# Optimization experiments

Measured on AMD Instinct MI355X. Metric: run time of the kernel, lower is better.

Reference implementation:

```python
import jax, jax.numpy as jnp
import numpy as np

N, E = 10000, 320000
IN_CH, HID, HEADS, OUT_CH = 128, 64, 4, 64
NEG_SLOPE = 0.2


def gat_conv(x, edge_index, edge_attr, W, a_src, a_dst, a_edge, W_edge, bias,
             heads, out_ch, concat):
    """PyG-style GATConv with edge_dim features.
    x: [N, F_in], edge_index: [2, E] (row0=src, row1=dst), edge_attr: [E, edge_dim].
    W: [F_in, heads*out_ch], a_*: [heads, out_ch], W_edge: [edge_dim, heads*out_ch],
    bias: [heads*out_ch] if concat else [out_ch].
    """
    n = x.shape[0]
    xh = (x @ W).reshape(n, heads, out_ch)                       # [N,H,C]
    src, dst = edge_index[0], edge_index[1]
    al_s = jnp.einsum('nhc,hc->nh', xh, a_src)                   # [N,H]
    al_d = jnp.einsum('nhc,hc->nh', xh, a_dst)                   # [N,H]
    eh = (edge_attr @ W_edge).reshape(-1, heads, out_ch)         # [E,H,C]
    al_e = jnp.einsum('ehc,hc->eh', eh, a_edge)                  # [E,H]
    alpha = jax.nn.leaky_relu(al_s[src] + al_d[dst] + al_e, NEG_SLOPE)  # [E,H]
    # segment softmax over incoming edges of each destination node
    amax = jax.ops.segment_max(alpha, dst, num_segments=n)       # [N,H]
    amax = jax.lax.stop_gradient(jnp.where(jnp.isfinite(amax), amax, 0.0))
    ex = jnp.exp(alpha - amax[dst])
    denom = jax.ops.segment_sum(ex, dst, num_segments=n)         # [N,H]
    att = ex / (denom[dst] + 1e-16)                              # [E,H]
    out = jax.ops.segment_sum(xh[src] * att[:, :, None], dst, num_segments=n)  # [N,H,C]
    out = out.reshape(n, heads * out_ch) if concat else out.mean(axis=1)
    return out + bias


def setup_inputs() -> dict:
    key = jax.random.key(0)
    ks = jax.random.split(key, 16)
    s1 = 1.0 / np.sqrt(IN_CH)
    s2 = 1.0 / np.sqrt(HEADS * HID)
    return {
        'x': jax.random.normal(ks[0], (N, IN_CH), dtype=jnp.float32),
        'edge_weight': jax.random.uniform(ks[1], (E, 1), dtype=jnp.float32),
        'W1': jax.random.normal(ks[2], (IN_CH, HEADS * HID), dtype=jnp.float32) * s1,
        'a_src1': jax.random.normal(ks[3], (HEADS, HID), dtype=jnp.float32) * s2,
        'a_dst1': jax.random.normal(ks[4], (HEADS, HID), dtype=jnp.float32) * s2,
        'a_edge1': jax.random.normal(ks[5], (HEADS, HID), dtype=jnp.float32) * s2,
        'We1': jax.random.normal(ks[6], (1, HEADS * HID), dtype=jnp.float32),
        'b1': jnp.zeros((HEADS * HID,), dtype=jnp.float32),
        'W2': jax.random.normal(ks[7], (HEADS * HID, OUT_CH), dtype=jnp.float32) * s2,
        'a_src2': jax.random.normal(ks[8], (1, OUT_CH), dtype=jnp.float32) * s2,
        'a_dst2': jax.random.normal(ks[9], (1, OUT_CH), dtype=jnp.float32) * s2,
        'a_edge2': jax.random.normal(ks[10], (1, OUT_CH), dtype=jnp.float32) * s2,
        'We2': jax.random.normal(ks[11], (1, OUT_CH), dtype=jnp.float32),
        'b2': jnp.zeros((OUT_CH,), dtype=jnp.float32),
        'edge_index': jax.random.randint(ks[12], (2, E), 0, N, dtype=jnp.int64
                                         if jax.config.jax_enable_x64 else jnp.int32),
    }


def reference(x, edge_weight, W1, a_src1, a_dst1, a_edge1, We1, b1,
              W2, a_src2, a_dst2, a_edge2, We2, b2, edge_index):
    h = gat_conv(x, edge_index, edge_weight, W1, a_src1, a_dst1, a_edge1, We1, b1,
                 heads=HEADS, out_ch=HID, concat=True)
    h = jax.nn.elu(h)
    out = gat_conv(h, edge_index, edge_weight, W2, a_src2, a_dst2, a_edge2, We2, b2,
                   heads=1, out_ch=OUT_CH, concat=False)
    return out
```

## Files before the change

kernel.cpp:

```cpp
#include <hip/hip_runtime.h>

constexpr int N_NODES = 10000;
constexpr int N_EDGES = 320000;
constexpr int IN_CH   = 128;
constexpr int HID     = 64;
constexpr int HEADS   = 4;
constexpr int OUT_CH  = 64;
constexpr int F1      = HEADS * HID;
constexpr int CAP     = 128;
constexpr float NEG_SLOPE = 0.2f;
constexpr int GEMM_BLOCKS = (N_NODES + 31) / 32;
constexpr int HALF_E = N_EDGES / 2;


__global__ void k_init(int* __restrict__ cnt,
                       const float* __restrict__ We1, const float* __restrict__ ae1,
                       const float* __restrict__ We2, const float* __restrict__ ae2,
                       float* __restrict__ de) {
    int bid = blockIdx.x;
    if (bid < 40) {
        int i = bid * 256 + threadIdx.x;
        if (i < N_NODES) cnt[i] = 0;
        return;
    }
    int t = threadIdx.x;
    if (t < HEADS) {
        float s = 0.f;
        for (int c = 0; c < HID; ++c) s = fmaf(We1[t * HID + c], ae1[t * HID + c], s);
        de[t] = s;
    } else if (t == HEADS) {
        float s = 0.f;
        for (int c = 0; c < OUT_CH; ++c) s = fmaf(We2[c], ae2[c], s);
        de[HEADS] = s;
    }
}


__global__ __launch_bounds__(256) void k_gemm1(const float* __restrict__ x,
                                               const float* __restrict__ W,
                                               const float* __restrict__ a_src,
                                               const float* __restrict__ a_dst,
                                               float* __restrict__ xh1T,
                                               float* __restrict__ als4,
                                               float* __restrict__ ald4) {
    __shared__ float xs[32 * IN_CH];
    int tid = threadIdx.x;
    int row0 = blockIdx.x * 32;
    int nrows = N_NODES - row0; if (nrows > 32) nrows = 32;
    float4* xs4 = (float4*)xs;
    const float4* xg = (const float4*)(x + (size_t)row0 * IN_CH);
    #pragma unroll
    for (int j = 0; j < 4; ++j) {
        int idx = tid + j * 256;
        if ((idx >> 5) < nrows) xs4[idx] = xg[idx];
    }
    __syncthreads();
    int wv = tid >> 6;
    int lane = tid & 63;
    int col = lane * 4;
    int h = lane >> 4;
    int c = (lane & 15) * 4;
    float acc[8][4];
    #pragma unroll
    for (int m = 0; m < 8; ++m)
        #pragma unroll
        for (int j = 0; j < 4; ++j) acc[m][j] = 0.f;

    for (int k = 0; k < IN_CH; k += 4) {
        float4 w0 = *(const float4*)(W + (size_t)(k + 0) * F1 + col);
        float4 w1 = *(const float4*)(W + (size_t)(k + 1) * F1 + col);
        float4 w2 = *(const float4*)(W + (size_t)(k + 2) * F1 + col);
        float4 w3 = *(const float4*)(W + (size_t)(k + 3) * F1 + col);
        #pragma unroll
        for (int m = 0; m < 8; ++m) {
            float4 xv = *(const float4*)(xs + (wv * 8 + m) * IN_CH + k);
            acc[m][0] = fmaf(xv.x, w0.x, fmaf(xv.y, w1.x, fmaf(xv.z, w2.x, fmaf(xv.w, w3.x, acc[m][0]))));
            acc[m][1] = fmaf(xv.x, w0.y, fmaf(xv.y, w1.y, fmaf(xv.z, w2.y, fmaf(xv.w, w3.y, acc[m][1]))));
            acc[m][2] = fmaf(xv.x, w0.z, fmaf(xv.y, w1.z, fmaf(xv.z, w2.z, fmaf(xv.w, w3.z, acc[m][2]))));
            acc[m][3] = fmaf(xv.x, w0.w, fmaf(xv.y, w1.w, fmaf(xv.z, w2.w, fmaf(xv.w, w3.w, acc[m][3]))));
        }
    }
    float4 asv = *(const float4*)(a_src + h * HID + c);
    float4 adv = *(const float4*)(a_dst + h * HID + c);
    #pragma unroll
    for (int m = 0; m < 8; ++m) {
        int row = wv * 8 + m;
        if (row < nrows)
            *(float4*)(xh1T + ((size_t)h * N_NODES + row0 + row) * HID + c) = *(float4*)acc[m];
        float s = acc[m][0] * asv.x + acc[m][1] * asv.y + acc[m][2] * asv.z + acc[m][3] * asv.w;
        float d = acc[m][0] * adv.x + acc[m][1] * adv.y + acc[m][2] * adv.z + acc[m][3] * adv.w;
        #pragma unroll
        for (int off = 1; off < 16; off <<= 1) {
            s += __shfl_xor(s, off, 64);
            d += __shfl_xor(d, off, 64);
        }
        if ((lane & 15) == 0 && row < nrows) {
            als4[(size_t)(row0 + row) * HEADS + h] = s;
            ald4[(size_t)(row0 + row) * HEADS + h] = d;
        }
    }
}


__global__ void k_fill(const int* __restrict__ src, const int* __restrict__ dst,
                       const float* __restrict__ ew,
                       const float* __restrict__ als4, const float* __restrict__ ald4,
                       const float* __restrict__ de, int* __restrict__ cnt,
                       int2* __restrict__ sw_pad, float4* __restrict__ ex_pad4) {
    int e0 = blockIdx.x * 256 + threadIdx.x;
    int e1 = e0 + HALF_E;
    int s0 = src[e0], d0 = dst[e0];
    int s1 = src[e1], d1 = dst[e1];
    float w0 = ew[e0], w1 = ew[e1];
    int p0 = atomicAdd(&cnt[d0], 1);
    int p1 = atomicAdd(&cnt[d1], 1);
    float4 as0 = *(const float4*)(als4 + (size_t)s0 * HEADS);
    float4 as1 = *(const float4*)(als4 + (size_t)s1 * HEADS);
    float4 ad0 = *(const float4*)(ald4 + (size_t)d0 * HEADS);
    float4 ad1 = *(const float4*)(ald4 + (size_t)d1 * HEADS);
    float4 dv = *(const float4*)de;
    if (p0 < CAP) {
        size_t q = (size_t)d0 * CAP + p0;
        sw_pad[q] = make_int2(s0, __float_as_int(w0));
        float4 a;
        a.x = as0.x + ad0.x + w0 * dv.x;
        a.y = as0.y + ad0.y + w0 * dv.y;
        a.z = as0.z + ad0.z + w0 * dv.z;
        a.w = as0.w + ad0.w + w0 * dv.w;
        a.x = a.x > 0.f ? a.x : NEG_SLOPE * a.x;
        a.y = a.y > 0.f ? a.y : NEG_SLOPE * a.y;
        a.z = a.z > 0.f ? a.z : NEG_SLOPE * a.z;
        a.w = a.w > 0.f ? a.w : NEG_SLOPE * a.w;
        a.x = __expf(a.x); a.y = __expf(a.y); a.z = __expf(a.z); a.w = __expf(a.w);
        ex_pad4[q] = a;
    }
    if (p1 < CAP) {
        size_t q = (size_t)d1 * CAP + p1;
        sw_pad[q] = make_int2(s1, __float_as_int(w1));
        float4 a;
        a.x = as1.x + ad1.x + w1 * dv.x;
        a.y = as1.y + ad1.y + w1 * dv.y;
        a.z = as1.z + ad1.z + w1 * dv.z;
        a.w = as1.w + ad1.w + w1 * dv.w;
        a.x = a.x > 0.f ? a.x : NEG_SLOPE * a.x;
        a.y = a.y > 0.f ? a.y : NEG_SLOPE * a.y;
        a.z = a.z > 0.f ? a.z : NEG_SLOPE * a.z;
        a.w = a.w > 0.f ? a.w : NEG_SLOPE * a.w;
        a.x = __expf(a.x); a.y = __expf(a.y); a.z = __expf(a.z); a.w = __expf(a.w);
        ex_pad4[q] = a;
    }
}


__global__ __launch_bounds__(256) void k_agg1(
        const float* __restrict__ xh1T, const float4* __restrict__ ex_pad4,
        const int2* __restrict__ sw_pad, const int* __restrict__ cnt,
        const float* __restrict__ bias, float* __restrict__ h1) {
    int b = blockIdx.x;
    int slot8 = b & 7;
    int h = slot8 >> 1;
    int nb = (b >> 3) * 2 + (slot8 & 1);
    int node = nb * 4 + (threadIdx.x >> 6);
    int lane = threadIdx.x & 63;
    int es = lane >> 4;
    int c4 = (lane & 15) * 4;
    const float* xb  = xh1T + (size_t)h * N_NODES * HID;
    const float* exb = (const float*)(ex_pad4 + (size_t)node * CAP) + h;
    const int2*  sp  = sw_pad + (size_t)node * CAP;
    int n = cnt[node]; if (n > CAP) n = CAP;
    float4 acc = make_float4(0.f, 0.f, 0.f, 0.f);
    float den = 0.f;
    int i = es;
    for (; i + 4 < n; i += 8) {
        float e0 = exb[i * 4], e1 = exb[(i + 4) * 4];
        int s0 = sp[i].x, s1 = sp[i + 4].x;
        float4 x0 = *(const float4*)(xb + (size_t)s0 * HID + c4);
        float4 x1 = *(const float4*)(xb + (size_t)s1 * HID + c4);
        den += e0 + e1;
        acc.x = fmaf(e0, x0.x, fmaf(e1, x1.x, acc.x));
        acc.y = fmaf(e0, x0.y, fmaf(e1, x1.y, acc.y));
        acc.z = fmaf(e0, x0.z, fmaf(e1, x1.z, acc.z));
        acc.w = fmaf(e0, x0.w, fmaf(e1, x1.w, acc.w));
    }
    if (i < n) {
        float e0 = exb[i * 4];
        int s0 = sp[i].x;
        float4 x0 = *(const float4*)(xb + (size_t)s0 * HID + c4);
        den += e0;
        acc.x = fmaf(e0, x0.x, acc.x);
        acc.y = fmaf(e0, x0.y, acc.y);
        acc.z = fmaf(e0, x0.z, acc.z);
        acc.w = fmaf(e0, x0.w, acc.w);
    }
    #pragma unroll
    for (int off = 32; off >= 16; off >>= 1) {
        acc.x += __shfl_xor(acc.x, off, 64);
        acc.y += __shfl_xor(acc.y, off, 64);
        acc.z += __shfl_xor(acc.z, off, 64);
        acc.w += __shfl_xor(acc.w, off, 64);
        den   += __shfl_xor(den,   off, 64);
    }
    if (es == 0) {
        float inv = 1.f / (den + 1e-16f);
        int cb = h * HID + c4;
        float4 o;
        o.x = fmaf(acc.x, inv, bias[cb + 0]);
        o.y = fmaf(acc.y, inv, bias[cb + 1]);
        o.z = fmaf(acc.z, inv, bias[cb + 2]);
        o.w = fmaf(acc.w, inv, bias[cb + 3]);
        o.x = o.x > 0.f ? o.x : expm1f(o.x);
        o.y = o.y > 0.f ? o.y : expm1f(o.y);
        o.z = o.z > 0.f ? o.z : expm1f(o.z);
        o.w = o.w > 0.f ? o.w : expm1f(o.w);
        *(float4*)(h1 + (size_t)node * F1 + cb) = o;
    }
}


__global__ __launch_bounds__(256) void k_gemm2(const float* __restrict__ hin,
                                               const float* __restrict__ W,
                                               const float* __restrict__ a_src,
                                               const float* __restrict__ a_dst,
                                               float* __restrict__ xh2,
                                               float* __restrict__ als,
                                               float* __restrict__ ald) {
    __shared__ float hs[32 * F1];
    int tid = threadIdx.x;
    int row0 = blockIdx.x * 32;
    int nrows = N_NODES - row0; if (nrows > 32) nrows = 32;
    float4* hs4 = (float4*)hs;
    const float4* hg = (const float4*)(hin + (size_t)row0 * F1);
    #pragma unroll
    for (int j = 0; j < 8; ++j) {
        int idx = tid + j * 256;
        if ((idx >> 6) < nrows) hs4[idx] = hg[idx];
    }
    __syncthreads();
    int rowg = tid >> 4;
    int col = (tid & 15) * 4;
    float acc[2][4];
    #pragma unroll
    for (int m = 0; m < 2; ++m)
        #pragma unroll
        for (int j = 0; j < 4; ++j) acc[m][j] = 0.f;
    for (int k = 0; k < F1; k += 4) {
        float4 w0 = *(const float4*)(W + (size_t)(k + 0) * OUT_CH + col);
        float4 w1 = *(const float4*)(W + (size_t)(k + 1) * OUT_CH + col);
        float4 w2 = *(const float4*)(W + (size_t)(k + 2) * OUT_CH + col);
        float4 w3 = *(const float4*)(W + (size_t)(k + 3) * OUT_CH + col);
        #pragma unroll
        for (int m = 0; m < 2; ++m) {
            float4 xv = *(const float4*)(hs + (rowg * 2 + m) * F1 + k);
            acc[m][0] = fmaf(xv.x, w0.x, fmaf(xv.y, w1.x, fmaf(xv.z, w2.x, fmaf(xv.w, w3.x, acc[m][0]))));
            acc[m][1] = fmaf(xv.x, w0.y, fmaf(xv.y, w1.y, fmaf(xv.z, w2.y, fmaf(xv.w, w3.y, acc[m][1]))));
            acc[m][2] = fmaf(xv.x, w0.z, fmaf(xv.y, w1.z, fmaf(xv.z, w2.z, fmaf(xv.w, w3.z, acc[m][2]))));
            acc[m][3] = fmaf(xv.x, w0.w, fmaf(xv.y, w1.w, fmaf(xv.z, w2.w, fmaf(xv.w, w3.w, acc[m][3]))));
        }
    }
    int lane = tid & 63;
    float4 asv = *(const float4*)(a_src + col);
    float4 adv = *(const float4*)(a_dst + col);
    #pragma unroll
    for (int m = 0; m < 2; ++m) {
        int row = rowg * 2 + m;
        if (row < nrows) *(float4*)(xh2 + (size_t)(row0 + row) * OUT_CH + col) = *(float4*)acc[m];
        float s = acc[m][0] * asv.x + acc[m][1] * asv.y + acc[m][2] * asv.z + acc[m][3] * asv.w;
        float d = acc[m][0] * adv.x + acc[m][1] * adv.y + acc[m][2] * adv.z + acc[m][3] * adv.w;
        #pragma unroll
        for (int off = 1; off < 16; off <<= 1) {
            s += __shfl_xor(s, off, 64);
            d += __shfl_xor(d, off, 64);
        }
        if ((lane & 15) == 0 && row < nrows) {
            als[row0 + row] = s;
            ald[row0 + row] = d;
        }
    }
}


__global__ __launch_bounds__(256) void k_agg2(
        const float* __restrict__ xh2, const float* __restrict__ als,
        const float* __restrict__ ald, const int2* __restrict__ sw_pad,
        const int* __restrict__ cnt, const float* __restrict__ de,
        const float* __restrict__ bias, float* __restrict__ out) {
    int node = blockIdx.x * 4 + (threadIdx.x >> 6);
    int lane = threadIdx.x & 63;
    int es = lane >> 4;
    int c4 = (lane & 15) * 4;
    float de2  = de[HEADS];
    float aldv = ald[node];
    const int2* sp = sw_pad + (size_t)node * CAP;
    int n = cnt[node]; if (n > CAP) n = CAP;
    float4 acc = make_float4(0.f, 0.f, 0.f, 0.f);
    float den = 0.f;
    int i = es;
    for (; i + 4 < n; i += 8) {
        int2 sw0 = sp[i], sw1 = sp[i + 4];
        int s0 = sw0.x, s1 = sw1.x;
        float w0 = __int_as_float(sw0.y), w1 = __int_as_float(sw1.y);
        float a0 = als[s0] + aldv + w0 * de2;
        float a1 = als[s1] + aldv + w1 * de2;
        a0 = a0 > 0.f ? a0 : NEG_SLOPE * a0;
        a1 = a1 > 0.f ? a1 : NEG_SLOPE * a1;
        float e0 = __expf(a0), e1 = __expf(a1);
        float4 x0 = *(const float4*)(xh2 + (size_t)s0 * OUT_CH + c4);
        float4 x1 = *(const float4*)(xh2 + (size_t)s1 * OUT_CH + c4);
        den += e0 + e1;
        acc.x = fmaf(e0, x0.x, fmaf(e1, x1.x, acc.x));
        acc.y = fmaf(e0, x0.y, fmaf(e1, x1.y, acc.y));
        acc.z = fmaf(e0, x0.z, fmaf(e1, x1.z, acc.z));
        acc.w = fmaf(e0, x0.w, fmaf(e1, x1.w, acc.w));
    }
    if (i < n) {
        int2 sw0 = sp[i];
        int s0 = sw0.x;
        float w0 = __int_as_float(sw0.y);
        float a0 = als[s0] + aldv + w0 * de2;
        a0 = a0 > 0.f ? a0 : NEG_SLOPE * a0;
        float e0 = __expf(a0);
        float4 x0 = *(const float4*)(xh2 + (size_t)s0 * OUT_CH + c4);
        den += e0;
        acc.x = fmaf(e0, x0.x, acc.x);
        acc.y = fmaf(e0, x0.y, acc.y);
        acc.z = fmaf(e0, x0.z, acc.z);
        acc.w = fmaf(e0, x0.w, acc.w);
    }
    #pragma unroll
    for (int off = 32; off >= 16; off >>= 1) {
        acc.x += __shfl_xor(acc.x, off, 64);
        acc.y += __shfl_xor(acc.y, off, 64);
        acc.z += __shfl_xor(acc.z, off, 64);
        acc.w += __shfl_xor(acc.w, off, 64);
        den   += __shfl_xor(den,   off, 64);
    }
    if (es == 0) {
        float inv = 1.f / (den + 1e-16f);
        float4 o;
        o.x = fmaf(acc.x, inv, bias[c4 + 0]);
        o.y = fmaf(acc.y, inv, bias[c4 + 1]);
        o.z = fmaf(acc.z, inv, bias[c4 + 2]);
        o.w = fmaf(acc.w, inv, bias[c4 + 3]);
        *(float4*)(out + (size_t)node * OUT_CH + c4) = o;
    }
}


extern "C" void kernel_launch(void* const* d_in, const int* in_sizes, int n_in,
                              void* d_out, int out_size, void* d_ws, size_t ws_size,
                              hipStream_t stream) {
    const float* x       = (const float*)d_in[0];
    const float* ew      = (const float*)d_in[1];
    const float* W1      = (const float*)d_in[2];
    const float* a_src1  = (const float*)d_in[3];
    const float* a_dst1  = (const float*)d_in[4];
    const float* a_edge1 = (const float*)d_in[5];
    const float* We1     = (const float*)d_in[6];
    const float* b1      = (const float*)d_in[7];
    const float* W2      = (const float*)d_in[8];
    const float* a_src2  = (const float*)d_in[9];
    const float* a_dst2  = (const float*)d_in[10];
    const float* a_edge2 = (const float*)d_in[11];
    const float* We2     = (const float*)d_in[12];
    const float* b2      = (const float*)d_in[13];
    const int*   eidx    = (const int*)d_in[14];
    const int* esrc = eidx;
    const int* edst = eidx + N_EDGES;
    float* out = (float*)d_out;

    char* p = (char*)d_ws;
    auto alloc = [&](size_t bytes) {
        char* r = p;
        p += (bytes + 255) & ~(size_t)255;
        return r;
    };
    float* xh1T     = (float*)alloc((size_t)N_NODES * F1 * 4);
    float* h1       = (float*)alloc((size_t)N_NODES * F1 * 4);
    float* xh2      = (float*)alloc((size_t)N_NODES * OUT_CH * 4);
    float* als4     = (float*)alloc((size_t)N_NODES * HEADS * 4);
    float* ald4     = (float*)alloc((size_t)N_NODES * HEADS * 4);
    float* als2     = (float*)alloc((size_t)N_NODES * 4);
    float* ald2     = (float*)alloc((size_t)N_NODES * 4);
    float* de       = (float*)alloc(8 * 4);
    int*   cnt      = (int*)alloc((size_t)N_NODES * 4);
    int2*  sw_pad   = (int2*)alloc((size_t)N_NODES * CAP * 8);
    float4* ex_pad4 = (float4*)alloc((size_t)N_NODES * CAP * 16);

    k_init<<<41, 256, 0, stream>>>(cnt, We1, a_edge1, We2, a_edge2, de);

    k_gemm1<<<GEMM_BLOCKS, 256, 0, stream>>>(x, W1, a_src1, a_dst1, xh1T, als4, ald4);

    k_fill<<<HALF_E / 256, 256, 0, stream>>>(esrc, edst, ew, als4, ald4, de,
                                             cnt, sw_pad, ex_pad4);

    k_agg1<<<N_NODES / 4 * HEADS, 256, 0, stream>>>(xh1T, ex_pad4, sw_pad, cnt, b1, h1);

    k_gemm2<<<GEMM_BLOCKS, 256, 0, stream>>>(h1, W2, a_src2, a_dst2, xh2, als2, ald2);
    k_agg2<<<N_NODES / 4, 256, 0, stream>>>(xh2, als2, ald2, sw_pad, cnt, de, b2, out);
}
```

Before: 121.7 us.

## Compute layer-1 attention exponentials inside aggregation instead of precomputing per edge

Result: no change. 121.7 us (+0.1%).

```diff
diff --git a/kernel.cpp b/kernel.cpp
--- a/kernel.cpp
+++ b/kernel.cpp
@@ -36,13 +36,28 @@
 }
 
 
+__global__ void k_fill(const int* __restrict__ src, const int* __restrict__ dst,
+                       const float* __restrict__ ew,
+                       int* __restrict__ cnt, int2* __restrict__ sw_pad) {
+    int e0 = blockIdx.x * 256 + threadIdx.x;
+    int e1 = e0 + HALF_E;
+    int s0 = src[e0], d0 = dst[e0];
+    int s1 = src[e1], d1 = dst[e1];
+    float w0 = ew[e0], w1 = ew[e1];
+    int p0 = atomicAdd(&cnt[d0], 1);
+    int p1 = atomicAdd(&cnt[d1], 1);
+    if (p0 < CAP) sw_pad[(size_t)d0 * CAP + p0] = make_int2(s0, __float_as_int(w0));
+    if (p1 < CAP) sw_pad[(size_t)d1 * CAP + p1] = make_int2(s1, __float_as_int(w1));
+}
+
+
 __global__ __launch_bounds__(256) void k_gemm1(const float* __restrict__ x,
                                                const float* __restrict__ W,
                                                const float* __restrict__ a_src,
                                                const float* __restrict__ a_dst,
                                                float* __restrict__ xh1T,
-                                               float* __restrict__ als4,
-                                               float* __restrict__ ald4) {
+                                               float* __restrict__ alsT,
+                                               float* __restrict__ aldT) {
     __shared__ float xs[32 * IN_CH];
     int tid = threadIdx.x;
     int row0 = blockIdx.x * 32;
@@ -95,66 +110,17 @@
             d += __shfl_xor(d, off, 64);
         }
         if ((lane & 15) == 0 && row < nrows) {
-            als4[(size_t)(row0 + row) * HEADS + h] = s;
-            ald4[(size_t)(row0 + row) * HEADS + h] = d;
-        }
-    }
-}
-
-
-__global__ void k_fill(const int* __restrict__ src, const int* __restrict__ dst,
-                       const float* __restrict__ ew,
-                       const float* __restrict__ als4, const float* __restrict__ ald4,
-                       const float* __restrict__ de, int* __restrict__ cnt,
-                       int2* __restrict__ sw_pad, float4* __restrict__ ex_pad4) {
-    int e0 = blockIdx.x * 256 + threadIdx.x;
-    int e1 = e0 + HALF_E;
-    int s0 = src[e0], d0 = dst[e0];
-    int s1 = src[e1], d1 = dst[e1];
-    float w0 = ew[e0], w1 = ew[e1];
-    int p0 = atomicAdd(&cnt[d0], 1);
-    int p1 = atomicAdd(&cnt[d1], 1);
-    float4 as0 = *(const float4*)(als4 + (size_t)s0 * HEADS);
-    float4 as1 = *(const float4*)(als4 + (size_t)s1 * HEADS);
-    float4 ad0 = *(const float4*)(ald4 + (size_t)d0 * HEADS);
-    float4 ad1 = *(const float4*)(ald4 + (size_t)d1 * HEADS);
-    float4 dv = *(const float4*)de;
-    if (p0 < CAP) {
-        size_t q = (size_t)d0 * CAP + p0;
-        sw_pad[q] = make_int2(s0, __float_as_int(w0));
-        float4 a;
-        a.x = as0.x + ad0.x + w0 * dv.x;
-        a.y = as0.y + ad0.y + w0 * dv.y;
-        a.z = as0.z + ad0.z + w0 * dv.z;
-        a.w = as0.w + ad0.w + w0 * dv.w;
-        a.x = a.x > 0.f ? a.x : NEG_SLOPE * a.x;
-        a.y = a.y > 0.f ? a.y : NEG_SLOPE * a.y;
-        a.z = a.z > 0.f ? a.z : NEG_SLOPE * a.z;
-        a.w = a.w > 0.f ? a.w : NEG_SLOPE * a.w;
-        a.x = __expf(a.x); a.y = __expf(a.y); a.z = __expf(a.z); a.w = __expf(a.w);
-        ex_pad4[q] = a;
-    }
-    if (p1 < CAP) {
-        size_t q = (size_t)d1 * CAP + p1;
-        sw_pad[q] = make_int2(s1, __float_as_int(w1));
-        float4 a;
-        a.x = as1.x + ad1.x + w1 * dv.x;
-        a.y = as1.y + ad1.y + w1 * dv.y;
-        a.z = as1.z + ad1.z + w1 * dv.z;
-        a.w = as1.w + ad1.w + w1 * dv.w;
-        a.x = a.x > 0.f ? a.x : NEG_SLOPE * a.x;
-        a.y = a.y > 0.f ? a.y : NEG_SLOPE * a.y;
-        a.z = a.z > 0.f ? a.z : NEG_SLOPE * a.z;
-        a.w = a.w > 0.f ? a.w : NEG_SLOPE * a.w;
-        a.x = __expf(a.x); a.y = __expf(a.y); a.z = __expf(a.z); a.w = __expf(a.w);
-        ex_pad4[q] = a;
+            alsT[(size_t)h * N_NODES + row0 + row] = s;
+            aldT[(size_t)h * N_NODES + row0 + row] = d;
+        }
     }
 }
 
 
 __global__ __launch_bounds__(256) void k_agg1(
-        const float* __restrict__ xh1T, const float4* __restrict__ ex_pad4,
-        const int2* __restrict__ sw_pad, const int* __restrict__ cnt,
+        const float* __restrict__ xh1T, const float* __restrict__ alsT,
+        const float* __restrict__ aldT, const int2* __restrict__ sw_pad,
+        const int* __restrict__ cnt, const float* __restrict__ de,
         const float* __restrict__ bias, float* __restrict__ h1) {
     int b = blockIdx.x;
     int slot8 = b & 7;
@@ -164,28 +130,44 @@
     int lane = threadIdx.x & 63;
     int es = lane >> 4;
     int c4 = (lane & 15) * 4;
-    const float* xb  = xh1T + (size_t)h * N_NODES * HID;
-    const float* exb = (const float*)(ex_pad4 + (size_t)node * CAP) + h;
-    const int2*  sp  = sw_pad + (size_t)node * CAP;
+    const float* xb   = xh1T + (size_t)h * N_NODES * HID;
+    const float* alsb = alsT + (size_t)h * N_NODES;
+    float deh  = de[h];
+    float aldv = aldT[(size_t)h * N_NODES + node];
+    const int2* sp = sw_pad + (size_t)node * CAP;
     int n = cnt[node]; if (n > CAP) n = CAP;
     float4 acc = make_float4(0.f, 0.f, 0.f, 0.f);
     float den = 0.f;
     int i = es;
-    for (; i + 4 < n; i += 8) {
-        float e0 = exb[i * 4], e1 = exb[(i + 4) * 4];
-        int s0 = sp[i].x, s1 = sp[i + 4].x;
-        float4 x0 = *(const float4*)(xb + (size_t)s0 * HID + c4);
-        float4 x1 = *(const float4*)(xb + (size_t)s1 * HID + c4);
-        den += e0 + e1;
-        acc.x = fmaf(e0, x0.x, fmaf(e1, x1.x, acc.x));
-        acc.y = fmaf(e0, x0.y, fmaf(e1, x1.y, acc.y));
-        acc.z = fmaf(e0, x0.z, fmaf(e1, x1.z, acc.z));
-        acc.w = fmaf(e0, x0.w, fmaf(e1, x1.w, acc.w));
-    }
-    if (i < n) {
-        float e0 = exb[i * 4];
-        int s0 = sp[i].x;
-        float4 x0 = *(const float4*)(xb + (size_t)s0 * HID + c4);
+    for (; i + 12 < n; i += 16) {
+        int2 r0 = sp[i], r1 = sp[i + 4], r2 = sp[i + 8], r3 = sp[i + 12];
+        float al0 = alsb[r0.x], al1 = alsb[r1.x], al2 = alsb[r2.x], al3 = alsb[r3.x];
+        float4 x0 = *(const float4*)(xb + (size_t)r0.x * HID + c4);
+        float4 x1 = *(const float4*)(xb + (size_t)r1.x * HID + c4);
+        float4 x2 = *(const float4*)(xb + (size_t)r2.x * HID + c4);
+        float4 x3 = *(const float4*)(xb + (size_t)r3.x * HID + c4);
+        float a0 = al0 + aldv + __int_as_float(r0.y) * deh;
+        float a1 = al1 + aldv + __int_as_float(r1.y) * deh;
+        float a2 = al2 + aldv + __int_as_float(r2.y) * deh;
+        float a3 = al3 + aldv + __int_as_float(r3.y) * deh;
+        a0 = a0 > 0.f ? a0 : NEG_SLOPE * a0;
+        a1 = a1 > 0.f ? a1 : NEG_SLOPE * a1;
+        a2 = a2 > 0.f ? a2 : NEG_SLOPE * a2;
+        a3 = a3 > 0.f ? a3 : NEG_SLOPE * a3;
+        float e0 = __expf(a0), e1 = __expf(a1), e2 = __expf(a2), e3 = __expf(a3);
+        den += (e0 + e1) + (e2 + e3);
+        acc.x = fmaf(e0, x0.x, fmaf(e1, x1.x, fmaf(e2, x2.x, fmaf(e3, x3.x, acc.x))));
+        acc.y = fmaf(e0, x0.y, fmaf(e1, x1.y, fmaf(e2, x2.y, fmaf(e3, x3.y, acc.y))));
+        acc.z = fmaf(e0, x0.z, fmaf(e1, x1.z, fmaf(e2, x2.z, fmaf(e3, x3.z, acc.z))));
+        acc.w = fmaf(e0, x0.w, fmaf(e1, x1.w, fmaf(e2, x2.w, fmaf(e3, x3.w, acc.w))));
+    }
+    for (; i < n; i += 4) {
+        int2 r0 = sp[i];
+        float al0 = alsb[r0.x];
+        float4 x0 = *(const float4*)(xb + (size_t)r0.x * HID + c4);
+        float a0 = al0 + aldv + __int_as_float(r0.y) * deh;
+        a0 = a0 > 0.f ? a0 : NEG_SLOPE * a0;
+        float e0 = __expf(a0);
         den += e0;
         acc.x = fmaf(e0, x0.x, acc.x);
         acc.y = fmaf(e0, x0.y, acc.y);
@@ -295,31 +277,35 @@
     float4 acc = make_float4(0.f, 0.f, 0.f, 0.f);
     float den = 0.f;
     int i = es;
-    for (; i + 4 < n; i += 8) {
-        int2 sw0 = sp[i], sw1 = sp[i + 4];
-        int s0 = sw0.x, s1 = sw1.x;
-        float w0 = __int_as_float(sw0.y), w1 = __int_as_float(sw1.y);
-        float a0 = als[s0] + aldv + w0 * de2;
-        float a1 = als[s1] + aldv + w1 * de2;
+    for (; i + 12 < n; i += 16) {
+        int2 r0 = sp[i], r1 = sp[i + 4], r2 = sp[i + 8], r3 = sp[i + 12];
+        float al0 = als[r0.x], al1 = als[r1.x], al2 = als[r2.x], al3 = als[r3.x];
+        float4 x0 = *(const float4*)(xh2 + (size_t)r0.x * OUT_CH + c4);
+        float4 x1 = *(const float4*)(xh2 + (size_t)r1.x * OUT_CH + c4);
+        float4 x2 = *(const float4*)(xh2 + (size_t)r2.x * OUT_CH + c4);
+        float4 x3 = *(const float4*)(xh2 + (size_t)r3.x * OUT_CH + c4);
+        float a0 = al0 + aldv + __int_as_float(r0.y) * de2;
+        float a1 = al1 + aldv + __int_as_float(r1.y) * de2;
+        float a2 = al2 + aldv + __int_as_float(r2.y) * de2;
+        float a3 = al3 + aldv + __int_as_float(r3.y) * de2;
         a0 = a0 > 0.f ? a0 : NEG_SLOPE * a0;
         a1 = a1 > 0.f ? a1 : NEG_SLOPE * a1;
-        float e0 = __expf(a0), e1 = __expf(a1);
-        float4 x0 = *(const float4*)(xh2 + (size_t)s0 * OUT_CH + c4);
-        float4 x1 = *(const float4*)(xh2 + (size_t)s1 * OUT_CH + c4);
-        den += e0 + e1;
-        acc.x = fmaf(e0, x0.x, fmaf(e1, x1.x, acc.x));
-        acc.y = fmaf(e0, x0.y, fmaf(e1, x1.y, acc.y));
-        acc.z = fmaf(e0, x0.z, fmaf(e1, x1.z, acc.z));
-        acc.w = fmaf(e0, x0.w, fmaf(e1, x1.w, acc.w));
-    }
-    if (i < n) {
-        int2 sw0 = sp[i];
-        int s0 = sw0.x;
-        float w0 = __int_as_float(sw0.y);
-        float a0 = als[s0] + aldv + w0 * de2;
+        a2 = a2 > 0.f ? a2 : NEG_SLOPE * a2;
+        a3 = a3 > 0.f ? a3 : NEG_SLOPE * a3;
+        float e0 = __expf(a0), e1 = __expf(a1), e2 = __expf(a2), e3 = __expf(a3);
+        den += (e0 + e1) + (e2 + e3);
+        acc.x = fmaf(e0, x0.x, fmaf(e1, x1.x, fmaf(e2, x2.x, fmaf(e3, x3.x, acc.x))));
+        acc.y = fmaf(e0, x0.y, fmaf(e1, x1.y, fmaf(e2, x2.y, fmaf(e3, x3.y, acc.y))));
+        acc.z = fmaf(e0, x0.z, fmaf(e1, x1.z, fmaf(e2, x2.z, fmaf(e3, x3.z, acc.z))));
+        acc.w = fmaf(e0, x0.w, fmaf(e1, x1.w, fmaf(e3, x3.w, fmaf(e2, x2.w, acc.w))));
+    }
+    for (; i < n; i += 4) {
+        int2 r0 = sp[i];
+        float al0 = als[r0.x];
+        float4 x0 = *(const float4*)(xh2 + (size_t)r0.x * OUT_CH + c4);
+        float a0 = al0 + aldv + __int_as_float(r0.y) * de2;
         a0 = a0 > 0.f ? a0 : NEG_SLOPE * a0;
         float e0 = __expf(a0);
-        float4 x0 = *(const float4*)(xh2 + (size_t)s0 * OUT_CH + c4);
         den += e0;
         acc.x = fmaf(e0, x0.x, acc.x);
         acc.y = fmaf(e0, x0.y, acc.y);
@@ -374,26 +360,25 @@
         p += (bytes + 255) & ~(size_t)255;
         return r;
     };
-    float* xh1T     = (float*)alloc((size_t)N_NODES * F1 * 4);
-    float* h1       = (float*)alloc((size_t)N_NODES * F1 * 4);
-    float* xh2      = (float*)alloc((size_t)N_NODES * OUT_CH * 4);
-    float* als4     = (float*)alloc((size_t)N_NODES * HEADS * 4);
-    float* ald4     = (float*)alloc((size_t)N_NODES * HEADS * 4);
-    float* als2     = (float*)alloc((size_t)N_NODES * 4);
-    float* ald2     = (float*)alloc((size_t)N_NODES * 4);
-    float* de       = (float*)alloc(8 * 4);
-    int*   cnt      = (int*)alloc((size_t)N_NODES * 4);
-    int2*  sw_pad   = (int2*)alloc((size_t)N_NODES * CAP * 8);
-    float4* ex_pad4 = (float4*)alloc((size_t)N_NODES * CAP * 16);
+    float* xh1T   = (float*)alloc((size_t)N_NODES * F1 * 4);
+    float* h1     = (float*)alloc((size_t)N_NODES * F1 * 4);
+    float* xh2    = (float*)alloc((size_t)N_NODES * OUT_CH * 4);
+    float* alsT   = (float*)alloc((size_t)N_NODES * HEADS * 4);
+    float* aldT   = (float*)alloc((size_t)N_NODES * HEADS * 4);
+    float* als2   = (float*)alloc((size_t)N_NODES * 4);
+    float* ald2   = (float*)alloc((size_t)N_NODES * 4);
+    float* de     = (float*)alloc(8 * 4);
+    int*   cnt    = (int*)alloc((size_t)N_NODES * 4);
+    int2*  sw_pad = (int2*)alloc((size_t)N_NODES * CAP * 8);
 
     k_init<<<41, 256, 0, stream>>>(cnt, We1, a_edge1, We2, a_edge2, de);
 
-    k_gemm1<<<GEMM_BLOCKS, 256, 0, stream>>>(x, W1, a_src1, a_dst1, xh1T, als4, ald4);
-
-    k_fill<<<HALF_E / 256, 256, 0, stream>>>(esrc, edst, ew, als4, ald4, de,
-                                             cnt, sw_pad, ex_pad4);
-
-    k_agg1<<<N_NODES / 4 * HEADS, 256, 0, stream>>>(xh1T, ex_pad4, sw_pad, cnt, b1, h1);
+    k_fill<<<HALF_E / 256, 256, 0, stream>>>(esrc, edst, ew, cnt, sw_pad);
+
+    k_gemm1<<<GEMM_BLOCKS, 256, 0, stream>>>(x, W1, a_src1, a_dst1, xh1T, alsT, aldT);
+
+    k_agg1<<<N_NODES / 4 * HEADS, 256, 0, stream>>>(
+        xh1T, alsT, aldT, sw_pad, cnt, de, b1, h1);
 
     k_gemm2<<<GEMM_BLOCKS, 256, 0, stream>>>(h1, W2, a_src2, a_dst2, xh2, als2, ald2);
     k_agg2<<<N_NODES / 4, 256, 0, stream>>>(xh2, als2, ald2, sw_pad, cnt, de, b2, out);
```
